# Optimization experiments

Hardware: AMD Instinct MI355X
Metric: run time of the kernel (lower is better)

## Reference

```python
import jax, jax.numpy as jnp
import numpy as np

B, C, H, W = 16, 64, 64, 64
C1, C2 = 8, 32  # block_channels_1 = C/8, block_channels_2 = C/2


def _conv1x1(x, w, b):
    # x: [B,C,H,W], w: [O,C] (1x1 kernel), b: [O]
    return jnp.einsum('bchw,oc->bohw', x, w) + b[None, :, None, None]


def _maxpool2(x):
    # MaxPool2d(kernel_size=2): window 2x2, stride 2, no padding
    return jax.lax.reduce_window(x, -jnp.inf, jax.lax.max,
                                 (1, 1, 2, 2), (1, 1, 2, 2), 'VALID')


def setup_inputs() -> dict:
    key = jax.random.key(0)
    ks = jax.random.split(key, 10)
    s = lambda fan_in: 1.0 / np.sqrt(fan_in)
    return {
        'nonlocal_input': jax.random.normal(ks[0], (B, C, H, W), jnp.float32),
        # spectral-normalized conv weights are treated as the effective (already
        # normalized) weights; 1x1 kernels stored as [out, in]
        'w_delta': jax.random.normal(ks[1], (C1, C), jnp.float32) * s(C),
        'b_delta': jax.random.normal(ks[2], (C1,), jnp.float32) * 0.01,
        'w_phi': jax.random.normal(ks[3], (C1, C), jnp.float32) * s(C),
        'b_phi': jax.random.normal(ks[4], (C1,), jnp.float32) * 0.01,
        'w_g': jax.random.normal(ks[5], (C2, C), jnp.float32) * s(C),
        'b_g': jax.random.normal(ks[6], (C2,), jnp.float32) * 0.01,
        'w_last': jax.random.normal(ks[7], (C, C2), jnp.float32) * s(C2),
        'b_last': jax.random.normal(ks[8], (C,), jnp.float32) * 0.01,
        # torch init is zeros; use a nonzero value so the attention path matters
        'gamma': jnp.asarray([0.7], jnp.float32),
    }


def reference(nonlocal_input, w_delta, b_delta, w_phi, b_phi, w_g, b_g,
              w_last, b_last, gamma):
    x = nonlocal_input
    b, c, h, w = x.shape

    # delta: [B,C1,H,W] -> [B, HW, C1]
    delta = _conv1x1(x, w_delta, b_delta)
    delta = jnp.transpose(delta, (0, 2, 3, 1)).reshape(b, h * w, C1)

    # phi: conv + pool -> [B,C1,H/2,W/2]; NOTE: the original permutes
    # (1,0,2,3) BEFORE reshaping to [B, C1, HW/4] (faithful to source).
    phi = _maxpool2(_conv1x1(x, w_phi, b_phi))
    phi = jnp.transpose(phi, (1, 0, 2, 3)).reshape(b, C1, -1)

    # attention: [B, HW, HW/4]
    attn = jax.nn.softmax(jnp.einsum('bnk,bkm->bnm', delta, phi), axis=-1)

    # g: conv + pool -> [B, HW/4, C2]
    g = _maxpool2(_conv1x1(x, w_g, b_g))
    g = jnp.transpose(g, (0, 2, 3, 1)).reshape(b, -1, C2)

    out = jnp.einsum('bnm,bmc->bnc', attn, g)          # [B, HW, C2]
    out = out.reshape(b, h, w, C2).transpose(0, 3, 1, 2)  # [B, C2, H, W]

    return gamma[0] * _conv1x1(out, w_last, b_last) + x
```

## Files before the change

kernel.cpp:

```cpp
#include <hip/hip_runtime.h>
#include <hip/hip_bf16.h>
#include <math.h>

typedef __attribute__((ext_vector_type(8))) short bf16x8;
typedef __attribute__((ext_vector_type(4))) float f32x4;

#define B_   16
#define C_   64
#define C1_  8
#define C2_  32
#define HW_  4096
#define M_   1024
#define LOG2E 1.4426950408889634f
#define MFMA_BF16 __builtin_amdgcn_mfma_f32_16x16x32_bf16

__device__ __forceinline__ unsigned short f2bf(float f) {
  union { float f; unsigned u; } v; v.f = f;
  unsigned r = (v.u + 0x7fffu + ((v.u >> 16) & 1u)) >> 16;
  return (unsigned short)r;
}
__device__ __forceinline__ float bf2f(unsigned short h) {
  union { unsigned u; float f; } v; v.u = ((unsigned)h) << 16;
  return v.f;
}

__global__ __launch_bounds__(256, 4)
void k_pre(const float* __restrict__ x,
           const float* __restrict__ w_phi, const float* __restrict__ b_phi,
           const float* __restrict__ w_g,   const float* __restrict__ b_g,
           unsigned short* __restrict__ phi_s,
           unsigned short* __restrict__ g_t) {
  __shared__ float comb[2*64*41];
  int tid = threadIdx.x;

  int qt  = tid >> 6;
  int sub = tid & 63;
  int id  = blockIdx.x * 64 + sub;
  int pix = id & 3;
  int pm  = id >> 2;
  int b = pm >> 10;
  int m = pm & 1023;
  int py = 2*(m >> 5) + (pix >> 1);
  int px = 2*(m & 31) + (pix & 1);
  int n = py * 64 + px;

  int c0 = __builtin_amdgcn_readfirstlane(qt << 4);

  const float* xp = x + ((size_t)b*C_ + c0)*HW_ + n;
  float xv[16];
  #pragma unroll
  for (int i = 0; i < 16; ++i) xv[i] = xp[(size_t)i * HW_];

  float ap[8], ag[32];
  #pragma unroll
  for (int o = 0; o < 8; ++o) {
    const float* wp = w_phi + o*C_ + c0;
    float a = 0.f;
    #pragma unroll
    for (int i = 0; i < 16; ++i) a += xv[i]*wp[i];
    ap[o] = a;
  }
  #pragma unroll
  for (int o = 0; o < 32; ++o) {
    const float* wg = w_g + o*C_ + c0;
    float a = 0.f;
    #pragma unroll
    for (int i = 0; i < 16; ++i) a += xv[i]*wg[i];
    ag[o] = a;
  }

  if (qt == 1 || qt == 3) {
    float* cb = comb + (((qt >> 1)*64) + sub)*41;
    #pragma unroll
    for (int o = 0; o < 8; ++o) cb[o] = ap[o];
    #pragma unroll
    for (int o = 0; o < 32; ++o) cb[8+o] = ag[o];
  }
  __syncthreads();
  if (qt == 0 || qt == 2) {
    const float* cb = comb + (((qt >> 1)*64) + sub)*41;
    #pragma unroll
    for (int o = 0; o < 8; ++o) ap[o] += cb[o];
    #pragma unroll
    for (int o = 0; o < 32; ++o) ag[o] += cb[8+o];
  }
  __syncthreads();
  if (qt == 2) {
    float* cb = comb + sub*41;
    #pragma unroll
    for (int o = 0; o < 8; ++o) cb[o] = ap[o];
    #pragma unroll
    for (int o = 0; o < 32; ++o) cb[8+o] = ag[o];
  }
  __syncthreads();
  if (qt == 0) {
    const float* cb = comb + sub*41;
    #pragma unroll
    for (int o = 0; o < 8; ++o) ap[o] += cb[o];
    #pragma unroll
    for (int o = 0; o < 32; ++o) ag[o] += cb[8+o];

    #pragma unroll
    for (int o = 0; o < 8; ++o) {
      float v = ap[o];
      v = fmaxf(v, __shfl_xor(v, 1));
      v = fmaxf(v, __shfl_xor(v, 2));
      ap[o] = v;
    }
    #pragma unroll
    for (int o = 0; o < 32; ++o) {
      float v = ag[o];
      v = fmaxf(v, __shfl_xor(v, 1));
      v = fmaxf(v, __shfl_xor(v, 2));
      ag[o] = v;
    }

    if ((sub & 3) == 0) {
      #pragma unroll
      for (int cp = 0; cp < 8; ++cp) {
        int f = cp*16 + b;
        float v = ap[cp] + b_phi[cp];
        unsigned short hi = f2bf(v);
        unsigned short* pr = phi_s + ((size_t)(f >> 3)*M_ + m)*16;
        pr[f & 7]       = hi;
        pr[8 + (f & 7)] = f2bf(v - bf2f(hi));
      }
      #pragma unroll
      for (int o = 0; o < 32; ++o)
        g_t[((size_t)b*C2_ + o)*M_ + m] = f2bf(ag[o] + b_g[o]);
    }
  }
}

__global__ __launch_bounds__(512, 4)
void k_attn(const float* __restrict__ x,
            const float* __restrict__ w_delta,
            const float* __restrict__ b_delta,
            const unsigned short* __restrict__ phi_s,
            const unsigned short* __restrict__ g_t,
            const float* __restrict__ w_last,
            const float* __restrict__ b_last,
            const float* __restrict__ gamma,
            float* __restrict__ out) {
  __shared__ __align__(16) unsigned char lds_raw[50176];
  __shared__ __align__(8)  unsigned short delta_lds[128*16];
  unsigned short* phi_lds = (unsigned short*)lds_raw;
  unsigned short* g_lds   = (unsigned short*)(lds_raw + 16384);
  float* o_sh = (float*)lds_raw;
  float* cmb  = (float*)(lds_raw + 16896);

  int tid  = threadIdx.x;
  int lane = tid & 63;
  int wv   = tid >> 6;
  int rg   = wv & 3;
  int kh   = wv >> 2;
  int r    = lane & 15;
  int q    = lane >> 4;
  int bx = blockIdx.x;
  int b  = bx >> 5;
  int n0 = (bx & 31) * 128;

  {
    int row  = tid & 127;
    int cp2  = __builtin_amdgcn_readfirstlane(tid >> 7);
    const float* wd0 = w_delta + (2*cp2)   * C_;
    const float* wd1 = w_delta + (2*cp2+1) * C_;
    const float* xr  = x + (size_t)b*C_*HW_ + n0 + row;
    float a0 = 0.f, a1 = 0.f;
    #pragma unroll
    for (int c = 0; c < C_; ++c) {
      float v = xr[(size_t)c * HW_];
      a0 += v * wd0[c];
      a1 += v * wd1[c];
    }
    a0 = (a0 + b_delta[2*cp2])   * LOG2E;
    a1 = (a1 + b_delta[2*cp2+1]) * LOG2E;
    unsigned short h0 = f2bf(a0), h1 = f2bf(a1);
    unsigned short l0 = f2bf(a0 - bf2f(h0)), l1 = f2bf(a1 - bf2f(h1));
    *(unsigned*)(delta_lds + row*16 + 2*cp2)     = (unsigned)h0 | ((unsigned)h1 << 16);
    *(unsigned*)(delta_lds + row*16 + 8 + 2*cp2) = (unsigned)l0 | ((unsigned)l1 << 16);
  }
  __syncthreads();

  bf16x8 df[2];
  #pragma unroll
  for (int t = 0; t < 2; ++t)
    df[t] = *(const bf16x8*)(delta_lds + (rg*32 + t*16 + r)*16 + (q & 1)*8);

  int phi_off = (q >> 1) * 8;
  int key0 = (r >> 2)*8 + (r & 3);
  int key1 = key0 + 4;

  bf16x8 ones;
  #pragma unroll
  for (int i = 0; i < 8; ++i) ones[i] = (short)0x3F80;

  f32x4 acc[2][2];
  f32x4 den[2];
  f32x4 zero = {0,0,0,0};
  #pragma unroll
  for (int t = 0; t < 2; ++t) { acc[t][0] = zero; acc[t][1] = zero; den[t] = zero; }

  for (int p = 0; p < 2; ++p) {
    if (p) __syncthreads();
    {
      const uint4* psrc = (const uint4*)(phi_s + ((size_t)b*M_ + p*512)*16);
      uint4* pdst = (uint4*)phi_lds;
      #pragma unroll
      for (int u = 0; u < 2; ++u) pdst[tid + u*512] = psrc[tid + u*512];
      #pragma unroll
      for (int u = 0; u < 4; ++u) {
        int uu = tid + u*512;
        int c2 = uu >> 6, pos = uu & 63;
        *(uint4*)(g_lds + c2*520 + pos*8) =
            *(const uint4*)(g_t + ((size_t)b*C2_ + c2)*M_ + p*512 + pos*8);
      }
    }
    __syncthreads();

    #pragma unroll 2
    for (int kc = 0; kc < 256; kc += 32) {
      int kl = kh*256 + kc;
      bf16x8 aphi0 = *(const bf16x8*)(phi_lds + (size_t)(kl + key0)*16 + phi_off);
      bf16x8 aphi1 = *(const bf16x8*)(phi_lds + (size_t)(kl + key1)*16 + phi_off);
      bf16x8 bg0   = *(const bf16x8*)(g_lds + r*520        + kl + q*8);
      bf16x8 bg1   = *(const bf16x8*)(g_lds + (16 + r)*520 + kl + q*8);

      #pragma unroll
      for (int t = 0; t < 2; ++t) {
        f32x4 s0 = MFMA_BF16(aphi0, df[t], zero, 0, 0, 0);
        f32x4 s1 = MFMA_BF16(aphi1, df[t], zero, 0, 0, 0);
        union { bf16x8 v; __hip_bfloat162 h[4]; } e;
        e.h[0] = __float22bfloat162_rn(make_float2(__builtin_amdgcn_exp2f(s0[0]),
                                                   __builtin_amdgcn_exp2f(s0[1])));
        e.h[1] = __float22bfloat162_rn(make_float2(__builtin_amdgcn_exp2f(s0[2]),
                                                   __builtin_amdgcn_exp2f(s0[3])));
        e.h[2] = __float22bfloat162_rn(make_float2(__builtin_amdgcn_exp2f(s1[0]),
                                                   __builtin_amdgcn_exp2f(s1[1])));
        e.h[3] = __float22bfloat162_rn(make_float2(__builtin_amdgcn_exp2f(s1[2]),
                                                   __builtin_amdgcn_exp2f(s1[3])));
        acc[t][0] = MFMA_BF16(e.v, bg0, acc[t][0], 0, 0, 0);
        acc[t][1] = MFMA_BF16(e.v, bg1, acc[t][1], 0, 0, 0);
        den[t]    = MFMA_BF16(e.v, ones, den[t], 0, 0, 0);
      }
    }
  }

  __syncthreads();
  if (kh == 1) {
    #pragma unroll
    for (int t = 0; t < 2; ++t) {
      #pragma unroll
      for (int reg = 0; reg < 4; ++reg) {
        int row = rg*32 + t*16 + q*4 + reg;
        cmb[row*34 + r]      = acc[t][0][reg];
        cmb[row*34 + 16 + r] = acc[t][1][reg];
        if (r == 0) cmb[row*34 + 32] = den[t][reg];
      }
    }
  }
  __syncthreads();
  if (kh == 0) {
    #pragma unroll
    for (int t = 0; t < 2; ++t) {
      #pragma unroll
      for (int reg = 0; reg < 4; ++reg) {
        int row = rg*32 + t*16 + q*4 + reg;
        float o0 = acc[t][0][reg] + cmb[row*34 + r];
        float o1 = acc[t][1][reg] + cmb[row*34 + 16 + r];
        float dn = den[t][reg]    + cmb[row*34 + 32];
        float iv = __builtin_amdgcn_rcpf(dn);
        o_sh[row*33 + r]      = o0 * iv;
        o_sh[row*33 + 16 + r] = o1 * iv;
      }
    }
  }
  __syncthreads();

  int rr  = tid & 127;
  int wqu = __builtin_amdgcn_readfirstlane(tid >> 7);
  float o_reg[32];
  #pragma unroll
  for (int c = 0; c < 32; ++c) o_reg[c] = o_sh[rr*33 + c];
  float gm = gamma[0];
  for (int i = 0; i < 16; ++i) {
    int co = wqu*16 + i;
    const float* wl = w_last + co*32;
    float a = b_last[co];
    #pragma unroll
    for (int c = 0; c < 32; ++c) a += wl[c] * o_reg[c];
    size_t oi = ((size_t)b*C_ + co)*HW_ + (size_t)(n0 + rr);
    out[oi] = gm * a + x[oi];
  }
}

extern "C" void kernel_launch(void* const* d_in, const int* in_sizes, int n_in,
                              void* d_out, int out_size, void* d_ws, size_t ws_size,
                              hipStream_t stream) {
  const float* x       = (const float*)d_in[0];
  const float* w_delta = (const float*)d_in[1];
  const float* b_delta = (const float*)d_in[2];
  const float* w_phi   = (const float*)d_in[3];
  const float* b_phi   = (const float*)d_in[4];
  const float* w_g     = (const float*)d_in[5];
  const float* b_g     = (const float*)d_in[6];
  const float* w_last  = (const float*)d_in[7];
  const float* b_last  = (const float*)d_in[8];
  const float* gamma   = (const float*)d_in[9];
  float* out = (float*)d_out;

  unsigned short* ws = (unsigned short*)d_ws;
  unsigned short* phi_s = ws;
  unsigned short* g_t   = ws + (size_t)B_*M_*16;

  hipLaunchKernelGGL(k_pre, dim3(1024), dim3(256), 0, stream,
                     x, w_phi, b_phi, w_g, b_g, phi_s, g_t);
  hipLaunchKernelGGL(k_attn, dim3(512), dim3(512), 0, stream,
                     x, w_delta, b_delta, phi_s, g_t, w_last, b_last, gamma, out);
}
```

Measured before the change: 114.6 us.

## Halve attention block to 256 threads with 64-row waves and register prefetch of second phase

Each block now uses 4 waves instead of 8, so each wave handles 64 query rows (four 16-row tiles) and reuses every phi/g fragment loaded from LDS across twice as many MFMAs. The second half of phi and g is prefetched from global memory into registers before the first phase computes, which overlaps that load with compute instead of stalling between phases. The trade-off is more register pressure (larger accumulators plus the prefetch buffers), half as many threads per block, and twice the epilogue work per thread.

```diff
diff --git a/kernel.cpp b/kernel.cpp
--- a/kernel.cpp
+++ b/kernel.cpp
@@ -132,7 +132,7 @@
   }
 }
 
-__global__ __launch_bounds__(512, 4)
+__global__ __launch_bounds__(256, 2)
 void k_attn(const float* __restrict__ x,
             const float* __restrict__ w_delta,
             const float* __restrict__ b_delta,
@@ -152,8 +152,8 @@
   int tid  = threadIdx.x;
   int lane = tid & 63;
   int wv   = tid >> 6;
-  int rg   = wv & 3;
-  int kh   = wv >> 2;
+  int rg   = wv & 1;
+  int kh   = wv >> 1;
   int r    = lane & 15;
   int q    = lane >> 4;
   int bx = blockIdx.x;
@@ -161,31 +161,36 @@
   int n0 = (bx & 31) * 128;
 
   {
-    int row  = tid & 127;
-    int cp2  = __builtin_amdgcn_readfirstlane(tid >> 7);
-    const float* wd0 = w_delta + (2*cp2)   * C_;
-    const float* wd1 = w_delta + (2*cp2+1) * C_;
-    const float* xr  = x + (size_t)b*C_*HW_ + n0 + row;
-    float a0 = 0.f, a1 = 0.f;
+    int row = tid & 127;
+    int hf  = __builtin_amdgcn_readfirstlane(tid >> 7);
+    const float* xr = x + (size_t)b*C_*HW_ + n0 + row;
+    float a[4] = {0.f, 0.f, 0.f, 0.f};
     #pragma unroll
     for (int c = 0; c < C_; ++c) {
       float v = xr[(size_t)c * HW_];
-      a0 += v * wd0[c];
-      a1 += v * wd1[c];
-    }
-    a0 = (a0 + b_delta[2*cp2])   * LOG2E;
-    a1 = (a1 + b_delta[2*cp2+1]) * LOG2E;
-    unsigned short h0 = f2bf(a0), h1 = f2bf(a1);
-    unsigned short l0 = f2bf(a0 - bf2f(h0)), l1 = f2bf(a1 - bf2f(h1));
-    *(unsigned*)(delta_lds + row*16 + 2*cp2)     = (unsigned)h0 | ((unsigned)h1 << 16);
-    *(unsigned*)(delta_lds + row*16 + 8 + 2*cp2) = (unsigned)l0 | ((unsigned)l1 << 16);
-  }
-  __syncthreads();
-
-  bf16x8 df[2];
-  #pragma unroll
-  for (int t = 0; t < 2; ++t)
-    df[t] = *(const bf16x8*)(delta_lds + (rg*32 + t*16 + r)*16 + (q & 1)*8);
+      #pragma unroll
+      for (int j = 0; j < 4; ++j) a[j] += v * w_delta[(4*hf + j)*C_ + c];
+    }
+    unsigned short h[4], l[4];
+    #pragma unroll
+    for (int j = 0; j < 4; ++j) {
+      float v = (a[j] + b_delta[4*hf + j]) * LOG2E;
+      h[j] = f2bf(v);
+      l[j] = f2bf(v - bf2f(h[j]));
+    }
+    unsigned* dh = (unsigned*)(delta_lds + row*16 + 4*hf);
+    dh[0] = (unsigned)h[0] | ((unsigned)h[1] << 16);
+    dh[1] = (unsigned)h[2] | ((unsigned)h[3] << 16);
+    unsigned* dl = (unsigned*)(delta_lds + row*16 + 8 + 4*hf);
+    dl[0] = (unsigned)l[0] | ((unsigned)l[1] << 16);
+    dl[1] = (unsigned)l[2] | ((unsigned)l[3] << 16);
+  }
+  __syncthreads();
+
+  bf16x8 df[4];
+  #pragma unroll
+  for (int t = 0; t < 4; ++t)
+    df[t] = *(const bf16x8*)(delta_lds + (rg*64 + t*16 + r)*16 + (q & 1)*8);
 
   int phi_off = (q >> 1) * 8;
   int key0 = (r >> 2)*8 + (r & 3);
@@ -195,28 +200,53 @@
   #pragma unroll
   for (int i = 0; i < 8; ++i) ones[i] = (short)0x3F80;
 
-  f32x4 acc[2][2];
-  f32x4 den[2];
+  f32x4 acc[4][2];
+  f32x4 den[4];
   f32x4 zero = {0,0,0,0};
   #pragma unroll
-  for (int t = 0; t < 2; ++t) { acc[t][0] = zero; acc[t][1] = zero; den[t] = zero; }
+  for (int t = 0; t < 4; ++t) { acc[t][0] = zero; acc[t][1] = zero; den[t] = zero; }
+
+  {
+    const uint4* psrc = (const uint4*)(phi_s + (size_t)b*M_*16);
+    uint4* pdst = (uint4*)phi_lds;
+    #pragma unroll
+    for (int u = 0; u < 4; ++u) pdst[tid + u*256] = psrc[tid + u*256];
+    #pragma unroll
+    for (int u = 0; u < 8; ++u) {
+      int uu = tid + u*256;
+      int c2 = uu >> 6, pos = uu & 63;
+      *(uint4*)(g_lds + c2*520 + pos*8) =
+          *(const uint4*)(g_t + ((size_t)b*C2_ + c2)*M_ + pos*8);
+    }
+  }
+  uint4 pf_phi[4], pf_g[8];
+  {
+    const uint4* psrc = (const uint4*)(phi_s + ((size_t)b*M_ + 512)*16);
+    #pragma unroll
+    for (int u = 0; u < 4; ++u) pf_phi[u] = psrc[tid + u*256];
+    #pragma unroll
+    for (int u = 0; u < 8; ++u) {
+      int uu = tid + u*256;
+      int c2 = uu >> 6, pos = uu & 63;
+      pf_g[u] = *(const uint4*)(g_t + ((size_t)b*C2_ + c2)*M_ + 512 + pos*8);
+    }
+  }
+  __syncthreads();
 
   for (int p = 0; p < 2; ++p) {
-    if (p) __syncthreads();
-    {
-      const uint4* psrc = (const uint4*)(phi_s + ((size_t)b*M_ + p*512)*16);
+    if (p) {
+      __syncthreads();
       uint4* pdst = (uint4*)phi_lds;
       #pragma unroll
-      for (int u = 0; u < 2; ++u) pdst[tid + u*512] = psrc[tid + u*512];
-      #pragma unroll
-      for (int u = 0; u < 4; ++u) {
-        int uu = tid + u*512;
+      for (int u = 0; u < 4; ++u) pdst[tid + u*256] = pf_phi[u];
+      #pragma unroll
+      for (int u = 0; u < 8; ++u) {
+        int uu = tid + u*256;
         int c2 = uu >> 6, pos = uu & 63;
-        *(uint4*)(g_lds + c2*520 + pos*8) =
-            *(const uint4*)(g_t + ((size_t)b*C2_ + c2)*M_ + p*512 + pos*8);
-      }
-    }
-    __syncthreads();
+        *(uint4*)(g_lds + c2*520 + pos*8) = pf_g[u];
+      }
+      __syncthreads();
+    }
 
     #pragma unroll 2
     for (int kc = 0; kc < 256; kc += 32) {
@@ -227,7 +257,7 @@
       bf16x8 bg1   = *(const bf16x8*)(g_lds + (16 + r)*520 + kl + q*8);
 
       #pragma unroll
-      for (int t = 0; t < 2; ++t) {
+      for (int t = 0; t < 4; ++t) {
         f32x4 s0 = MFMA_BF16(aphi0, df[t], zero, 0, 0, 0);
         f32x4 s1 = MFMA_BF16(aphi1, df[t], zero, 0, 0, 0);
         union { bf16x8 v; __hip_bfloat162 h[4]; } e;
@@ -249,10 +279,10 @@
   __syncthreads();
   if (kh == 1) {
     #pragma unroll
-    for (int t = 0; t < 2; ++t) {
+    for (int t = 0; t < 4; ++t) {
       #pragma unroll
       for (int reg = 0; reg < 4; ++reg) {
-        int row = rg*32 + t*16 + q*4 + reg;
+        int row = rg*64 + t*16 + q*4 + reg;
         cmb[row*34 + r]      = acc[t][0][reg];
         cmb[row*34 + 16 + r] = acc[t][1][reg];
         if (r == 0) cmb[row*34 + 32] = den[t][reg];
@@ -262,10 +292,10 @@
   __syncthreads();
   if (kh == 0) {
     #pragma unroll
-    for (int t = 0; t < 2; ++t) {
+    for (int t = 0; t < 4; ++t) {
       #pragma unroll
       for (int reg = 0; reg < 4; ++reg) {
-        int row = rg*32 + t*16 + q*4 + reg;
+        int row = rg*64 + t*16 + q*4 + reg;
         float o0 = acc[t][0][reg] + cmb[row*34 + r];
         float o1 = acc[t][1][reg] + cmb[row*34 + 16 + r];
         float dn = den[t][reg]    + cmb[row*34 + 32];
@@ -283,8 +313,8 @@
   #pragma unroll
   for (int c = 0; c < 32; ++c) o_reg[c] = o_sh[rr*33 + c];
   float gm = gamma[0];
-  for (int i = 0; i < 16; ++i) {
-    int co = wqu*16 + i;
+  for (int i = 0; i < 32; ++i) {
+    int co = wqu*32 + i;
     const float* wl = w_last + co*32;
     float a = b_last[co];
     #pragma unroll
@@ -315,6 +345,6 @@
 
   hipLaunchKernelGGL(k_pre, dim3(1024), dim3(256), 0, stream,
                      x, w_phi, b_phi, w_g, b_g, phi_s, g_t);
-  hipLaunchKernelGGL(k_attn, dim3(512), dim3(512), 0, stream,
+  hipLaunchKernelGGL(k_attn, dim3(512), dim3(256), 0, stream,
                      x, w_delta, b_delta, phi_s, g_t, w_last, b_last, gamma, out);
 }
```

Measured after the change: 127.6 us. +11.4%, slower.

## Stream phi/g tiles in four chunks with register prefetch and smaller LDS

Applied to the files above, without the earlier changes.

The attention kernel now walks the key dimension in four chunks of 256 keys instead of two chunks of 512, so the LDS tile buffers roughly halve and launch bounds request 6 blocks per SM instead of 4. The next chunk's phi and g data are prefetched into registers while the current chunk is computed, then written to LDS between barriers, so global load latency overlaps MFMA work. In exchange there are more barriers per block and extra registers for the prefetch, which could work against the higher occupancy target. The o_sh/cmb epilogue buffers still use fixed offsets into the shrunk LDS region, which may be tight.

```diff
diff --git a/kernel.cpp b/kernel.cpp
--- a/kernel.cpp
+++ b/kernel.cpp
@@ -132,7 +132,7 @@
   }
 }
 
-__global__ __launch_bounds__(512, 4)
+__global__ __launch_bounds__(512, 6)
 void k_attn(const float* __restrict__ x,
             const float* __restrict__ w_delta,
             const float* __restrict__ b_delta,
@@ -142,10 +142,10 @@
             const float* __restrict__ b_last,
             const float* __restrict__ gamma,
             float* __restrict__ out) {
-  __shared__ __align__(16) unsigned char lds_raw[50176];
+  __shared__ __align__(16) unsigned char lds_raw[34304];
   __shared__ __align__(8)  unsigned short delta_lds[128*16];
   unsigned short* phi_lds = (unsigned short*)lds_raw;
-  unsigned short* g_lds   = (unsigned short*)(lds_raw + 16384);
+  unsigned short* g_lds   = (unsigned short*)(lds_raw + 8192);
   float* o_sh = (float*)lds_raw;
   float* cmb  = (float*)(lds_raw + 16896);
 
@@ -201,30 +201,46 @@
   #pragma unroll
   for (int t = 0; t < 2; ++t) { acc[t][0] = zero; acc[t][1] = zero; den[t] = zero; }
 
-  for (int p = 0; p < 2; ++p) {
-    if (p) __syncthreads();
-    {
-      const uint4* psrc = (const uint4*)(phi_s + ((size_t)b*M_ + p*512)*16);
-      uint4* pdst = (uint4*)phi_lds;
-      #pragma unroll
-      for (int u = 0; u < 2; ++u) pdst[tid + u*512] = psrc[tid + u*512];
-      #pragma unroll
-      for (int u = 0; u < 4; ++u) {
-        int uu = tid + u*512;
-        int c2 = uu >> 6, pos = uu & 63;
-        *(uint4*)(g_lds + c2*520 + pos*8) =
-            *(const uint4*)(g_t + ((size_t)b*C2_ + c2)*M_ + p*512 + pos*8);
-      }
-    }
-    __syncthreads();
+  int g_c2  = tid >> 5;
+  int g_pos = tid & 31;
+
+  {
+    ((uint4*)phi_lds)[tid] = ((const uint4*)(phi_s + (size_t)b*M_*16))[tid];
+    #pragma unroll
+    for (int u = 0; u < 2; ++u) {
+      int c2 = g_c2 + u*16;
+      *(uint4*)(g_lds + c2*264 + g_pos*8) =
+          *(const uint4*)(g_t + ((size_t)b*C2_ + c2)*M_ + g_pos*8);
+    }
+  }
+  uint4 pf_phi, pf_g0, pf_g1;
+  pf_phi = ((const uint4*)(phi_s + ((size_t)b*M_ + 256)*16))[tid];
+  pf_g0  = *(const uint4*)(g_t + ((size_t)b*C2_ + g_c2)*M_      + 256 + g_pos*8);
+  pf_g1  = *(const uint4*)(g_t + ((size_t)b*C2_ + g_c2 + 16)*M_ + 256 + g_pos*8);
+  __syncthreads();
+
+  for (int p = 0; p < 4; ++p) {
+    if (p) {
+      __syncthreads();
+      ((uint4*)phi_lds)[tid] = pf_phi;
+      *(uint4*)(g_lds + g_c2*264 + g_pos*8)        = pf_g0;
+      *(uint4*)(g_lds + (g_c2 + 16)*264 + g_pos*8) = pf_g1;
+      if (p < 3) {
+        int kb = (p + 1) * 256;
+        pf_phi = ((const uint4*)(phi_s + ((size_t)b*M_ + kb)*16))[tid];
+        pf_g0  = *(const uint4*)(g_t + ((size_t)b*C2_ + g_c2)*M_      + kb + g_pos*8);
+        pf_g1  = *(const uint4*)(g_t + ((size_t)b*C2_ + g_c2 + 16)*M_ + kb + g_pos*8);
+      }
+      __syncthreads();
+    }
 
     #pragma unroll 2
-    for (int kc = 0; kc < 256; kc += 32) {
-      int kl = kh*256 + kc;
+    for (int kc = 0; kc < 128; kc += 32) {
+      int kl = kh*128 + kc;
       bf16x8 aphi0 = *(const bf16x8*)(phi_lds + (size_t)(kl + key0)*16 + phi_off);
       bf16x8 aphi1 = *(const bf16x8*)(phi_lds + (size_t)(kl + key1)*16 + phi_off);
-      bf16x8 bg0   = *(const bf16x8*)(g_lds + r*520        + kl + q*8);
-      bf16x8 bg1   = *(const bf16x8*)(g_lds + (16 + r)*520 + kl + q*8);
+      bf16x8 bg0   = *(const bf16x8*)(g_lds + r*264        + kl + q*8);
+      bf16x8 bg1   = *(const bf16x8*)(g_lds + (16 + r)*264 + kl + q*8);
 
       #pragma unroll
       for (int t = 0; t < 2; ++t) {
```

Result: slower. 122.0 us (+6.5%).

## Rewrite pre-kernel as lane-per-output-channel and pad/swizzle phi layout in LDS

Applied to the files above, without the earlier changes.

The pre-pass kernel now gives each lane one output channel (8 phi plus 32 g) with its weight row held in registers, and loops over pooled pixels using wave-uniform x loads. This replaces the four-way channel split that needed an LDS cross-wave reduction and shuffle-based pooling. Phi rows are written in a permuted slot order and padded from 16 to 24 shorts in LDS, and the attention kernel's key indexing is adjusted to match, to cut LDS bank conflicts on the phi fragment reads. The cost is more LDS per block, 64 weight registers per lane, 24 of 64 lanes idle, and scalar global stores in the pre-pass.

```diff
diff --git a/kernel.cpp b/kernel.cpp
--- a/kernel.cpp
+++ b/kernel.cpp
@@ -24,110 +24,58 @@
   return v.f;
 }
 
+__device__ __forceinline__ int slot32(int m) {
+  return (m & 0xFFE0) | (((m & 7) << 2) | ((m >> 3) & 3));
+}
+
 __global__ __launch_bounds__(256, 4)
 void k_pre(const float* __restrict__ x,
            const float* __restrict__ w_phi, const float* __restrict__ b_phi,
            const float* __restrict__ w_g,   const float* __restrict__ b_g,
            unsigned short* __restrict__ phi_s,
            unsigned short* __restrict__ g_t) {
-  __shared__ float comb[2*64*41];
-  int tid = threadIdx.x;
-
-  int qt  = tid >> 6;
-  int sub = tid & 63;
-  int id  = blockIdx.x * 64 + sub;
-  int pix = id & 3;
-  int pm  = id >> 2;
-  int b = pm >> 10;
-  int m = pm & 1023;
-  int py = 2*(m >> 5) + (pix >> 1);
-  int px = 2*(m & 31) + (pix & 1);
-  int n = py * 64 + px;
-
-  int c0 = __builtin_amdgcn_readfirstlane(qt << 4);
-
-  const float* xp = x + ((size_t)b*C_ + c0)*HW_ + n;
-  float xv[16];
-  #pragma unroll
-  for (int i = 0; i < 16; ++i) xv[i] = xp[(size_t)i * HW_];
-
-  float ap[8], ag[32];
-  #pragma unroll
-  for (int o = 0; o < 8; ++o) {
-    const float* wp = w_phi + o*C_ + c0;
-    float a = 0.f;
-    #pragma unroll
-    for (int i = 0; i < 16; ++i) a += xv[i]*wp[i];
-    ap[o] = a;
-  }
-  #pragma unroll
-  for (int o = 0; o < 32; ++o) {
-    const float* wg = w_g + o*C_ + c0;
-    float a = 0.f;
-    #pragma unroll
-    for (int i = 0; i < 16; ++i) a += xv[i]*wg[i];
-    ag[o] = a;
-  }
-
-  if (qt == 1 || qt == 3) {
-    float* cb = comb + (((qt >> 1)*64) + sub)*41;
-    #pragma unroll
-    for (int o = 0; o < 8; ++o) cb[o] = ap[o];
-    #pragma unroll
-    for (int o = 0; o < 32; ++o) cb[8+o] = ag[o];
-  }
-  __syncthreads();
-  if (qt == 0 || qt == 2) {
-    const float* cb = comb + (((qt >> 1)*64) + sub)*41;
-    #pragma unroll
-    for (int o = 0; o < 8; ++o) ap[o] += cb[o];
-    #pragma unroll
-    for (int o = 0; o < 32; ++o) ag[o] += cb[8+o];
-  }
-  __syncthreads();
-  if (qt == 2) {
-    float* cb = comb + sub*41;
-    #pragma unroll
-    for (int o = 0; o < 8; ++o) cb[o] = ap[o];
-    #pragma unroll
-    for (int o = 0; o < 32; ++o) cb[8+o] = ag[o];
-  }
-  __syncthreads();
-  if (qt == 0) {
-    const float* cb = comb + sub*41;
-    #pragma unroll
-    for (int o = 0; o < 8; ++o) ap[o] += cb[o];
-    #pragma unroll
-    for (int o = 0; o < 32; ++o) ag[o] += cb[8+o];
-
-    #pragma unroll
-    for (int o = 0; o < 8; ++o) {
-      float v = ap[o];
-      v = fmaxf(v, __shfl_xor(v, 1));
-      v = fmaxf(v, __shfl_xor(v, 2));
-      ap[o] = v;
-    }
-    #pragma unroll
-    for (int o = 0; o < 32; ++o) {
-      float v = ag[o];
-      v = fmaxf(v, __shfl_xor(v, 1));
-      v = fmaxf(v, __shfl_xor(v, 2));
-      ag[o] = v;
-    }
-
-    if ((sub & 3) == 0) {
-      #pragma unroll
-      for (int cp = 0; cp < 8; ++cp) {
-        int f = cp*16 + b;
-        float v = ap[cp] + b_phi[cp];
-        unsigned short hi = f2bf(v);
-        unsigned short* pr = phi_s + ((size_t)(f >> 3)*M_ + m)*16;
-        pr[f & 7]       = hi;
-        pr[8 + (f & 7)] = f2bf(v - bf2f(hi));
-      }
-      #pragma unroll
-      for (int o = 0; o < 32; ++o)
-        g_t[((size_t)b*C2_ + o)*M_ + m] = f2bf(ag[o] + b_g[o]);
+  int tid  = threadIdx.x;
+  int lane = tid & 63;
+  int wv   = tid >> 6;
+  int wave_id = blockIdx.x * 4 + wv;
+  int o  = lane;
+  int go = (o >= 8) ? ((o - 8 > 31) ? 31 : (o - 8)) : 0;
+
+  const float* wrow = (o < 8) ? (w_phi + o * C_) : (w_g + go * C_);
+  float w[64];
+  #pragma unroll
+  for (int v = 0; v < 16; ++v) {
+    float4 t = ((const float4*)wrow)[v];
+    w[4*v+0] = t.x; w[4*v+1] = t.y; w[4*v+2] = t.z; w[4*v+3] = t.w;
+  }
+  float bias = (o < 8) ? b_phi[o] : b_g[go];
+
+  #pragma unroll
+  for (int j = 0; j < 8; ++j) {
+    int pm = wave_id * 8 + j;
+    int b = pm >> 10;
+    int m = pm & 1023;
+    float pooled = -3.4e38f;
+    #pragma unroll
+    for (int pix = 0; pix < 4; ++pix) {
+      int n = (2*(m >> 5) + (pix >> 1)) * 64 + 2*(m & 31) + (pix & 1);
+      int xoff = __builtin_amdgcn_readfirstlane(b * C_ * HW_ + n);
+      const float* xp = x + xoff;
+      float cur = 0.f;
+      #pragma unroll
+      for (int c = 0; c < C_; ++c) cur += xp[(size_t)c * HW_] * w[c];
+      pooled = fmaxf(pooled, cur);
+    }
+    pooled += bias;
+
+    if (o < 8) {
+      int f = o * 16 + b;
+      unsigned short hi = f2bf(pooled);
+      unsigned short* pr = phi_s + ((size_t)(f >> 3) * M_ + slot32(m)) * 16;
+      pr[f & 7]       = hi;
+      pr[8 + (f & 7)] = f2bf(pooled - bf2f(hi));
+    } else if (o < 40) {
+      g_t[((size_t)b * C2_ + (o - 8)) * M_ + m] = f2bf(pooled);
     }
   }
 }
@@ -142,10 +90,10 @@
             const float* __restrict__ b_last,
             const float* __restrict__ gamma,
             float* __restrict__ out) {
-  __shared__ __align__(16) unsigned char lds_raw[50176];
+  __shared__ __align__(16) unsigned char lds_raw[57856];
   __shared__ __align__(8)  unsigned short delta_lds[128*16];
   unsigned short* phi_lds = (unsigned short*)lds_raw;
-  unsigned short* g_lds   = (unsigned short*)(lds_raw + 16384);
+  unsigned short* g_lds   = (unsigned short*)(lds_raw + 24576);
   float* o_sh = (float*)lds_raw;
   float* cmb  = (float*)(lds_raw + 16896);
 
@@ -188,8 +136,8 @@
     df[t] = *(const bf16x8*)(delta_lds + (rg*32 + t*16 + r)*16 + (q & 1)*8);
 
   int phi_off = (q >> 1) * 8;
-  int key0 = (r >> 2)*8 + (r & 3);
-  int key1 = key0 + 4;
+  int ks0 = ((r & 3) << 2) | (r >> 2);
+  int ks1 = ks0 + 16;
 
   bf16x8 ones;
   #pragma unroll
@@ -204,10 +152,10 @@
   for (int p = 0; p < 2; ++p) {
     if (p) __syncthreads();
     {
-      const uint4* psrc = (const uint4*)(phi_s + ((size_t)b*M_ + p*512)*16);
-      uint4* pdst = (uint4*)phi_lds;
-      #pragma unroll
-      for (int u = 0; u < 2; ++u) pdst[tid + u*512] = psrc[tid + u*512];
+      const uint4* src = (const uint4*)(phi_s + ((size_t)b*M_ + p*512 + tid)*16);
+      unsigned short* dst = phi_lds + tid*24;
+      ((uint4*)dst)[0] = src[0];
+      *(uint4*)(dst + 8) = src[1];
       #pragma unroll
       for (int u = 0; u < 4; ++u) {
         int uu = tid + u*512;
@@ -221,8 +169,8 @@
     #pragma unroll 2
     for (int kc = 0; kc < 256; kc += 32) {
       int kl = kh*256 + kc;
-      bf16x8 aphi0 = *(const bf16x8*)(phi_lds + (size_t)(kl + key0)*16 + phi_off);
-      bf16x8 aphi1 = *(const bf16x8*)(phi_lds + (size_t)(kl + key1)*16 + phi_off);
+      bf16x8 aphi0 = *(const bf16x8*)(phi_lds + (size_t)(kl + ks0)*24 + phi_off);
+      bf16x8 aphi1 = *(const bf16x8*)(phi_lds + (size_t)(kl + ks1)*24 + phi_off);
       bf16x8 bg0   = *(const bf16x8*)(g_lds + r*520        + kl + q*8);
       bf16x8 bg1   = *(const bf16x8*)(g_lds + (16 + r)*520 + kl + q*8);
 
@@ -313,7 +261,7 @@
   unsigned short* phi_s = ws;
   unsigned short* g_t   = ws + (size_t)B_*M_*16;
 
-  hipLaunchKernelGGL(k_pre, dim3(1024), dim3(256), 0, stream,
+  hipLaunchKernelGGL(k_pre, dim3(512), dim3(256), 0, stream,
                      x, w_phi, b_phi, w_g, b_g, phi_s, g_t);
   hipLaunchKernelGGL(k_attn, dim3(512), dim3(512), 0, stream,
                      x, w_delta, b_delta, phi_s, g_t, w_last, b_last, gamma, out);
```

After: 138.9 us. 1.21x slower.
